# Optimization experiments

Measured on AMD Instinct MI355X. Metric: run time of the kernel, lower is better.

## Reference

```python
import jax, jax.numpy as jnp
import numpy as np

N_PARTITIONS = 16
EPS = 1e-5


def setup_inputs() -> dict:
    key = jax.random.key(0)
    ks = jax.random.split(key, 8)
    B, in_size = 4096, 4096
    d = in_size // N_PARTITIONS  # 256
    s = 1.0 / np.sqrt(d)
    return {
        "x": jax.random.normal(ks[0], (B, in_size), dtype=jnp.float32),
        "WQ_w": jax.random.normal(ks[1], (d, d), dtype=jnp.float32) * s,
        "WQ_b": jax.random.normal(ks[2], (d,), dtype=jnp.float32) * s,
        "WK_w": jax.random.normal(ks[3], (d, d), dtype=jnp.float32) * s,
        "WK_b": jax.random.normal(ks[4], (d,), dtype=jnp.float32) * s,
        "WV_w": jax.random.normal(ks[5], (d, d), dtype=jnp.float32) * s,
        "WV_b": jax.random.normal(ks[6], (d,), dtype=jnp.float32) * s,
        "bn_gamma": jnp.ones((in_size,), dtype=jnp.float32),
        "bn_beta": jnp.zeros((in_size,), dtype=jnp.float32),
    }


def reference(x, WQ_w, WQ_b, WK_w, WK_b, WV_w, WV_b, bn_gamma, bn_beta):
    B, in_size = x.shape
    p = N_PARTITIONS
    d = in_size // p
    scale = jnp.asarray(np.sqrt(d), dtype=x.dtype)

    # BatchNorm1d in training mode: batch statistics, biased variance
    mean = jnp.mean(x, axis=0)
    var = jnp.mean((x - mean) ** 2, axis=0)
    x_norm = (x - mean) * jax.lax.rsqrt(var + EPS) * bn_gamma + bn_beta

    # Split features into partitions: [B, p, d]; shared Linear per partition.
    xp = x_norm.reshape(B, p, d)
    # Torch loop builds Q[b, :, i] = WQ(x_part_i)[b]  ->  [B, d, p]
    Q = jnp.einsum('bpd,ed->bep', xp, WQ_w) + WQ_b[None, :, None]
    K = jnp.einsum('bpd,ed->bep', xp, WK_w) + WK_b[None, :, None]
    V = jnp.einsum('bpd,ed->bep', xp, WV_w) + WV_b[None, :, None]

    # bmm(Q, K^T): [B, d, d], softmax over last axis, bmm with V: [B, d, p]
    dot = jnp.einsum('bep,bfp->bef', Q, K) / scale
    attn = jax.nn.softmax(dot, axis=2)
    prod = jnp.einsum('bef,bfp->bep', attn, V)

    # torch.cat(prod[:, i] for i in range(d), dim=1) == row-major flatten of [B, d, p]
    out = prod.reshape(B, d * p) + x
    return out
```

## Files before the change

kernel.cpp:

```cpp
#include <hip/hip_runtime.h>
#include <hip/hip_bf16.h>
#include <stdint.h>

typedef __attribute__((ext_vector_type(8))) short short8;
typedef __attribute__((ext_vector_type(4))) short short4_t;
typedef __attribute__((ext_vector_type(4))) float f32x4;
typedef __attribute__((ext_vector_type(2))) unsigned int u32x2;
typedef __attribute__((ext_vector_type(4))) unsigned int u32x4;

union FragU { u32x4 u; short8 s; };
union Frag2U { u32x2 u; short4_t s; };

__device__ __forceinline__ unsigned short f2bf(float f) {
  union { float f; uint32_t u; } v; v.f = f;
  uint32_t u = v.u;
  return (unsigned short)((u + 0x7FFFu + ((u >> 16) & 1u)) >> 16);
}

__device__ __forceinline__ unsigned pk2(float a, float b) {
  return (unsigned)f2bf(a) | ((unsigned)f2bf(b) << 16);
}

__device__ __forceinline__ void gload_lds16(const void* g, void* l) {
  __builtin_amdgcn_global_load_lds(
      (const __attribute__((address_space(1))) unsigned int*)g,
      (__attribute__((address_space(3))) unsigned int*)l, 16, 0, 0);
}

#if defined(__has_builtin)
#if __has_builtin(__builtin_amdgcn_mfma_f32_16x16x16bf16_1k)
#define HAVE_MFMA16_BUILTIN 1
#endif
#endif

__device__ __forceinline__ f32x4 mfma16(u32x2 a, u32x2 b, f32x4 c) {
#ifdef HAVE_MFMA16_BUILTIN
  Frag2U ua, ub;
  ua.u = a; ub.u = b;
  return __builtin_amdgcn_mfma_f32_16x16x16bf16_1k(ua.s, ub.s, c, 0, 0, 0);
#else
  asm volatile("s_nop 1\n\t"
               "v_mfma_f32_16x16x16_bf16 %0, %1, %2, %0\n\t"
               "s_nop 7\n\t"
               "s_nop 7"
               : "+v"(c) : "v"(a), "v"(b));
  return c;
#endif
}

__global__ __launch_bounds__(256) void k_wconv(const float* __restrict__ WQ,
                                               const float* __restrict__ WK,
                                               const float* __restrict__ WV,
                                               unsigned short* __restrict__ Wbf) {
  int mat = blockIdx.x >> 5;
  int i = blockIdx.x & 31;
  const float* W = (mat == 0) ? WQ : ((mat == 1) ? WK : WV);
  int off = i * 2048 + threadIdx.x * 8;
  f32x4 v0 = *(const f32x4*)(W + off), v1 = *(const f32x4*)(W + off + 4);
  u32x4 pk;
  pk.x = pk2(v0.x, v0.y); pk.y = pk2(v0.z, v0.w);
  pk.z = pk2(v1.x, v1.y); pk.w = pk2(v1.z, v1.w);
  *(u32x4*)(Wbf + (size_t)mat * 65536 + off) = pk;
}

__global__ __launch_bounds__(256) void k_stats(const float* __restrict__ x,
                                               float* __restrict__ psum,
                                               float* __restrict__ psq) {
  int t = threadIdx.x;
  int cb = blockIdx.x & 3;
  int ck = blockIdx.x >> 2;
  int c0 = cb * 1024 + t * 4;
  f32x4 s = {0.f, 0.f, 0.f, 0.f}, q = {0.f, 0.f, 0.f, 0.f};
  const float* base = x + (size_t)ck * 64 * 4096 + c0;
#pragma unroll 4
  for (int r = 0; r < 64; ++r) {
    f32x4 v = *(const f32x4*)(base + (size_t)r * 4096);
    s += v;
    q += v * v;
  }
  *(f32x4*)(psum + (size_t)ck * 4096 + c0) = s;
  *(f32x4*)(psq + (size_t)ck * 4096 + c0) = q;
}

__global__ __launch_bounds__(256) void k_finalize(const float* __restrict__ psum,
                                                  const float* __restrict__ psq,
                                                  const float* __restrict__ gamma,
                                                  const float* __restrict__ beta,
                                                  float* __restrict__ An,
                                                  float* __restrict__ Bn) {
  int c = blockIdx.x * 256 + threadIdx.x;
  float s = 0.f, q = 0.f;
  for (int k = 0; k < 64; ++k) {
    s += psum[k * 4096 + c];
    q += psq[k * 4096 + c];
  }
  float mean = s * (1.0f / 4096.0f);
  float var = q * (1.0f / 4096.0f) - mean * mean;
  float a = gamma[c] * rsqrtf(var + 1e-5f);
  An[c] = a;
  Bn[c] = beta[c] - mean * a;
}

__global__ __launch_bounds__(256) void k_qkv(
    const float* __restrict__ x, const float* __restrict__ An, const float* __restrict__ Bn,
    const unsigned short* __restrict__ Wbf,
    const float* __restrict__ bQ, const float* __restrict__ bK, const float* __restrict__ bV,
    unsigned short* __restrict__ Qt, unsigned short* __restrict__ Kt,
    unsigned short* __restrict__ Vo) {
  __shared__ unsigned short Asm[64 * 256];
  int t = threadIdx.x;
  int mb = blockIdx.x;

  for (int i = 0; i < 8; ++i) {
    int m = i * 8 + (t >> 5);
    int k0 = (t & 31) * 8;
    size_t r = (size_t)(mb * 64 + m);
    const float* xs = x + r * 256 + k0;
    f32x4 v0 = *(const f32x4*)(xs), v1 = *(const f32x4*)(xs + 4);
    int c = ((int)(r & 15)) * 256 + k0;
    f32x4 a0 = *(const f32x4*)(An + c), a1 = *(const f32x4*)(An + c + 4);
    f32x4 b0 = *(const f32x4*)(Bn + c), b1 = *(const f32x4*)(Bn + c + 4);
    f32x4 n0 = v0 * a0 + b0, n1 = v1 * a1 + b1;
    u32x4 pk;
    pk.x = pk2(n0.x, n0.y); pk.y = pk2(n0.z, n0.w);
    pk.z = pk2(n1.x, n1.y); pk.w = pk2(n1.z, n1.w);
    int off = m * 512 + ((k0 * 2) ^ ((m & 7) << 4));
    *(u32x4*)((char*)Asm + off) = pk;
  }
  __syncthreads();

  int w = t >> 6, ln = t & 63, lr = ln & 15, g = ln >> 4;
  int wn = w * 64;

#pragma unroll
  for (int mat = 0; mat < 3; ++mat) {
    const unsigned short* W = Wbf + (size_t)mat * 65536;
    const float* bias = (mat == 0) ? bQ : ((mat == 1) ? bK : bV);
    float scale = (mat == 0) ? 0.0625f : 1.0f;

    f32x4 acc[4][4];
    f32x4 z4 = {0.f, 0.f, 0.f, 0.f};
#pragma unroll
    for (int a_ = 0; a_ < 4; ++a_)
#pragma unroll
      for (int b_ = 0; b_ < 4; ++b_) acc[a_][b_] = z4;

#pragma unroll
    for (int kk = 0; kk < 8; ++kk) {
      FragU af[4], bfr[4];
#pragma unroll
      for (int nt = 0; nt < 4; ++nt) {
        int n = wn + nt * 16 + lr;
        bfr[nt].u = *(const u32x4*)((const char*)W + (size_t)n * 512 + kk * 64 + g * 16);
      }
#pragma unroll
      for (int mt = 0; mt < 4; ++mt) {
        int m = mt * 16 + lr;
        af[mt].u = *(const u32x4*)((const char*)Asm + m * 512 + ((kk * 64 + g * 16) ^ ((m & 7) << 4)));
      }
#pragma unroll
      for (int mt = 0; mt < 4; ++mt)
#pragma unroll
        for (int nt = 0; nt < 4; ++nt)
          acc[mt][nt] = __builtin_amdgcn_mfma_f32_16x16x32_bf16(af[mt].s, bfr[nt].s, acc[mt][nt], 0, 0, 0);
    }

#pragma unroll
    for (int nt = 0; nt < 4; ++nt) {
      int ccol = wn + nt * 16 + lr;
      float bvs = bias[ccol] * scale;
#pragma unroll
      for (int mt = 0; mt < 4; ++mt) {
        int rbase = mb * 64 + mt * 16;
        int b_ = rbase >> 4;
#pragma unroll
        for (int rg = 0; rg < 4; ++rg) {
          int p_ = g * 4 + rg;
          unsigned short val = f2bf(acc[mt][nt][rg] * scale + bvs);
          if (mat < 2) {
            (mat == 0 ? Qt : Kt)[(size_t)b_ * 4096 + (size_t)ccol * 16 + p_] = val;
          } else {
            Vo[(size_t)(rbase + p_) * 256 + ccol] = val;
          }
        }
      }
    }
  }
}

#define LQT 0
#define LKT 8192
#define LVS 16384
#define LTOT 24576

__global__ __launch_bounds__(256, 3) void k_attn(
    const unsigned short* __restrict__ Qtg, const unsigned short* __restrict__ Ktg,
    const unsigned short* __restrict__ Vg, const float* __restrict__ x,
    float* __restrict__ out) {
  __shared__ char lds[LTOT];
  int b = blockIdx.x;
  int t = threadIdx.x;
  int w = t >> 6, ln = t & 63, lr = ln & 15, g = ln >> 4;

  for (int i = w; i < 24; i += 4) {
    const unsigned short* srcmat;
    unsigned srcbyte;
    int region;
    if (i < 8) {
      srcmat = Qtg;
      srcbyte = (unsigned)b * 8192 + i * 1024 + ln * 16;
      region = LQT + i * 1024;
    } else if (i < 16) {
      int ii = i - 8;
      srcmat = Ktg;
      srcbyte = (unsigned)b * 8192 + ii * 1024 + ln * 16;
      region = LKT + ii * 1024;
    } else {
      int ii = i - 16;
      srcmat = Vg;
      int d = ii * 1024 + ln * 16;
      int p = d >> 9;
      int cc = d & 511;
      srcbyte = (unsigned)b * 8192 + p * 512 + (unsigned)(cc ^ ((p & 7) << 4));
      region = LVS + ii * 1024;
    }
    gload_lds16((const char*)srcmat + srcbyte, &lds[region]);
  }
  __syncthreads();

  u32x2 qf[4];
#pragma unroll
  for (int nt = 0; nt < 4; ++nt)
    qf[nt] = *(const u32x2*)(&lds[LQT + (w * 64 + nt * 16 + lr) * 32 + g * 8]);

  f32x4 accT[4];
  float denp[4];
  f32x4 z4 = {0.f, 0.f, 0.f, 0.f};
#pragma unroll
  for (int nt = 0; nt < 4; ++nt) { accT[nt] = z4; denp[nt] = 0.f; }

  for (int c = 0; c < 8; ++c) {
#pragma unroll
    for (int mt_ = 0; mt_ < 2; ++mt_) {
      u32x2 kf = *(const u32x2*)(&lds[LKT + (c * 32 + mt_ * 16 + lr) * 32 + g * 8]);

      f32x4 st[4];
#pragma unroll
      for (int nt = 0; nt < 4; ++nt)
        st[nt] = mfma16(kf, qf[nt], z4);

      u32x2 vf = *(const u32x2*)(
          &lds[LVS + lr * 512 + ((c * 64 + mt_ * 32 + g * 8) ^ ((lr & 7) << 4))]);

#pragma unroll
      for (int nt = 0; nt < 4; ++nt) {
        float e0 = __expf(st[nt].x);
        float e1 = __expf(st[nt].y);
        float e2 = __expf(st[nt].z);
        float e3 = __expf(st[nt].w);
        denp[nt] += (e0 + e1) + (e2 + e3);
        u32x2 pB;
        pB.x = pk2(e0, e1);
        pB.y = pk2(e2, e3);
        accT[nt] = mfma16(vf, pB, accT[nt]);
      }
    }
  }

#pragma unroll
  for (int nt = 0; nt < 4; ++nt) {
    float v = denp[nt];
    v += __shfl_xor(v, 16);
    v += __shfl_xor(v, 32);
    denp[nt] = v;
  }

  size_t rowbase = (size_t)b * 4096;
#pragma unroll
  for (int nt = 0; nt < 4; ++nt) {
    int e = w * 64 + nt * 16 + lr;
    size_t col = (size_t)e * 16 + g * 4;
    float inv = 1.0f / denp[nt];
    f32x4 xr = *(const f32x4*)(x + rowbase + col);
    f32x4 o = accT[nt] * inv + xr;
    *(f32x4*)(out + rowbase + col) = o;
  }
}

extern "C" void kernel_launch(void* const* d_in, const int* in_sizes, int n_in,
                              void* d_out, int out_size, void* d_ws, size_t ws_size,
                              hipStream_t stream) {
  const float* x = (const float*)d_in[0];
  const float* WQ = (const float*)d_in[1];
  const float* bQ = (const float*)d_in[2];
  const float* WK = (const float*)d_in[3];
  const float* bK = (const float*)d_in[4];
  const float* WV = (const float*)d_in[5];
  const float* bV = (const float*)d_in[6];
  const float* gamma = (const float*)d_in[7];
  const float* beta = (const float*)d_in[8];
  float* out = (float*)d_out;
  char* ws = (char*)d_ws;

  float* psum = (float*)(ws);
  float* psq = (float*)(ws + (1 << 20));
  float* An = (float*)(ws + (2 << 20));
  float* Bn = (float*)(ws + (2 << 20) + (16 << 10));
  unsigned short* Wbf = (unsigned short*)(ws + (3 << 20));
  unsigned short* Qt = (unsigned short*)(ws + (size_t)(4 << 20));
  unsigned short* Kt = (unsigned short*)(ws + (size_t)(4 << 20) + (32u << 20));
  unsigned short* Vo = (unsigned short*)(ws + (size_t)(4 << 20) + (64u << 20));

  hipLaunchKernelGGL(k_wconv, dim3(96), dim3(256), 0, stream, WQ, WK, WV, Wbf);
  hipLaunchKernelGGL(k_stats, dim3(256), dim3(256), 0, stream, x, psum, psq);
  hipLaunchKernelGGL(k_finalize, dim3(16), dim3(256), 0, stream, psum, psq, gamma, beta, An, Bn);
  hipLaunchKernelGGL(k_qkv, dim3(1024), dim3(256), 0, stream, x, An, Bn,
                     Wbf, bQ, bK, bV, Qt, Kt, Vo);
  hipLaunchKernelGGL(k_attn, dim3(4096), dim3(256), 0, stream, Qt, Kt, Vo, x, out);
}
```

Baseline: 153.2 us.

## Fuse QKV projection and attention into one per-wave kernel

Merges the QKV projection and attention kernels so each wave handles one batch row, keeping Q, K and V fragments in registers instead of writing them to global memory and reloading them through LDS. This removes the Q/K/V intermediate round trip (about 24 MB written and read back) and one kernel launch. The softmax exponent now uses exp2 with log2(e) folded into the Q scale. Each wave now reads all three weight matrices from global/L2 with no LDS sharing, and the register pressure is heavy (16-entry fragment arrays), which may cause spills or low occupancy.

```diff
diff --git a/kernel.cpp b/kernel.cpp
--- a/kernel.cpp
+++ b/kernel.cpp
@@ -21,17 +21,22 @@
   return (unsigned)f2bf(a) | ((unsigned)f2bf(b) << 16);
 }
 
-__device__ __forceinline__ void gload_lds16(const void* g, void* l) {
-  __builtin_amdgcn_global_load_lds(
-      (const __attribute__((address_space(1))) unsigned int*)g,
-      (__attribute__((address_space(3))) unsigned int*)l, 16, 0, 0);
-}
-
 #if defined(__has_builtin)
 #if __has_builtin(__builtin_amdgcn_mfma_f32_16x16x16bf16_1k)
 #define HAVE_MFMA16_BUILTIN 1
 #endif
-#endif
+#if __has_builtin(__builtin_amdgcn_exp2f)
+#define HAVE_EXP2_BUILTIN 1
+#endif
+#endif
+
+__device__ __forceinline__ float fexp2(float x) {
+#ifdef HAVE_EXP2_BUILTIN
+  return __builtin_amdgcn_exp2f(x);
+#else
+  return exp2f(x);
+#endif
+}
 
 __device__ __forceinline__ f32x4 mfma16(u32x2 a, u32x2 b, f32x4 c) {
 #ifdef HAVE_MFMA16_BUILTIN
@@ -101,186 +106,135 @@
   Bn[c] = beta[c] - mean * a;
 }
 
-__global__ __launch_bounds__(256) void k_qkv(
+__global__ __launch_bounds__(256, 2) void k_fused(
     const float* __restrict__ x, const float* __restrict__ An, const float* __restrict__ Bn,
     const unsigned short* __restrict__ Wbf,
     const float* __restrict__ bQ, const float* __restrict__ bK, const float* __restrict__ bV,
-    unsigned short* __restrict__ Qt, unsigned short* __restrict__ Kt,
-    unsigned short* __restrict__ Vo) {
-  __shared__ unsigned short Asm[64 * 256];
+    float* __restrict__ out) {
   int t = threadIdx.x;
-  int mb = blockIdx.x;
-
-  for (int i = 0; i < 8; ++i) {
-    int m = i * 8 + (t >> 5);
-    int k0 = (t & 31) * 8;
-    size_t r = (size_t)(mb * 64 + m);
-    const float* xs = x + r * 256 + k0;
-    f32x4 v0 = *(const f32x4*)(xs), v1 = *(const f32x4*)(xs + 4);
-    int c = ((int)(r & 15)) * 256 + k0;
+  int w = t >> 6, ln = t & 63, lr = ln & 15, g = ln >> 4;
+  int b = blockIdx.x * 4 + w;
+  const float* xrow = x + (size_t)b * 4096;
+
+  f32x4 z4 = {0.f, 0.f, 0.f, 0.f};
+
+  FragU af[8];
+#pragma unroll
+  for (int kk = 0; kk < 8; ++kk) {
+    int dd = kk * 32 + g * 8;
+    int c = lr * 256 + dd;
+    f32x4 v0 = *(const f32x4*)(xrow + c), v1 = *(const f32x4*)(xrow + c + 4);
     f32x4 a0 = *(const f32x4*)(An + c), a1 = *(const f32x4*)(An + c + 4);
     f32x4 b0 = *(const f32x4*)(Bn + c), b1 = *(const f32x4*)(Bn + c + 4);
     f32x4 n0 = v0 * a0 + b0, n1 = v1 * a1 + b1;
-    u32x4 pk;
-    pk.x = pk2(n0.x, n0.y); pk.y = pk2(n0.z, n0.w);
-    pk.z = pk2(n1.x, n1.y); pk.w = pk2(n1.z, n1.w);
-    int off = m * 512 + ((k0 * 2) ^ ((m & 7) << 4));
-    *(u32x4*)((char*)Asm + off) = pk;
-  }
-  __syncthreads();
-
-  int w = t >> 6, ln = t & 63, lr = ln & 15, g = ln >> 4;
-  int wn = w * 64;
-
-#pragma unroll
-  for (int mat = 0; mat < 3; ++mat) {
-    const unsigned short* W = Wbf + (size_t)mat * 65536;
-    const float* bias = (mat == 0) ? bQ : ((mat == 1) ? bK : bV);
-    float scale = (mat == 0) ? 0.0625f : 1.0f;
-
-    f32x4 acc[4][4];
-    f32x4 z4 = {0.f, 0.f, 0.f, 0.f};
-#pragma unroll
-    for (int a_ = 0; a_ < 4; ++a_)
-#pragma unroll
-      for (int b_ = 0; b_ < 4; ++b_) acc[a_][b_] = z4;
-
+    af[kk].u.x = pk2(n0.x, n0.y);
+    af[kk].u.y = pk2(n0.z, n0.w);
+    af[kk].u.z = pk2(n1.x, n1.y);
+    af[kk].u.w = pk2(n1.z, n1.w);
+  }
+
+  const char* WQp = (const char*)Wbf;
+  const char* WKp = (const char*)(Wbf + 65536);
+  const char* WVp = (const char*)(Wbf + 131072);
+
+  u32x2 qf[16];
+  {
+    f32x4 acc[16];
+#pragma unroll
+    for (int nt = 0; nt < 16; ++nt) acc[nt] = z4;
 #pragma unroll
     for (int kk = 0; kk < 8; ++kk) {
-      FragU af[4], bfr[4];
-#pragma unroll
-      for (int nt = 0; nt < 4; ++nt) {
-        int n = wn + nt * 16 + lr;
-        bfr[nt].u = *(const u32x4*)((const char*)W + (size_t)n * 512 + kk * 64 + g * 16);
+#pragma unroll
+      for (int nt = 0; nt < 16; ++nt) {
+        FragU bfr;
+        bfr.u = *(const u32x4*)(WQp + (size_t)(nt * 16 + lr) * 512 + kk * 64 + g * 16);
+        acc[nt] = __builtin_amdgcn_mfma_f32_16x16x32_bf16(af[kk].s, bfr.s, acc[nt], 0, 0, 0);
       }
-#pragma unroll
-      for (int mt = 0; mt < 4; ++mt) {
-        int m = mt * 16 + lr;
-        af[mt].u = *(const u32x4*)((const char*)Asm + m * 512 + ((kk * 64 + g * 16) ^ ((m & 7) << 4)));
+    }
+    const float QS = 0.0625f * 1.44269504088896f;
+#pragma unroll
+    for (int nt = 0; nt < 16; ++nt) {
+      float bq = bQ[nt * 16 + lr];
+      qf[nt].x = pk2((acc[nt][0] + bq) * QS, (acc[nt][1] + bq) * QS);
+      qf[nt].y = pk2((acc[nt][2] + bq) * QS, (acc[nt][3] + bq) * QS);
+    }
+  }
+
+  u32x2 kf[16];
+  {
+    f32x4 acc[16];
+#pragma unroll
+    for (int nt = 0; nt < 16; ++nt) acc[nt] = z4;
+#pragma unroll
+    for (int kk = 0; kk < 8; ++kk) {
+#pragma unroll
+      for (int nt = 0; nt < 16; ++nt) {
+        FragU bfr;
+        bfr.u = *(const u32x4*)(WKp + (size_t)(nt * 16 + lr) * 512 + kk * 64 + g * 16);
+        acc[nt] = __builtin_amdgcn_mfma_f32_16x16x32_bf16(af[kk].s, bfr.s, acc[nt], 0, 0, 0);
       }
-#pragma unroll
-      for (int mt = 0; mt < 4; ++mt)
-#pragma unroll
-        for (int nt = 0; nt < 4; ++nt)
-          acc[mt][nt] = __builtin_amdgcn_mfma_f32_16x16x32_bf16(af[mt].s, bfr[nt].s, acc[mt][nt], 0, 0, 0);
-    }
-
-#pragma unroll
-    for (int nt = 0; nt < 4; ++nt) {
-      int ccol = wn + nt * 16 + lr;
-      float bvs = bias[ccol] * scale;
-#pragma unroll
-      for (int mt = 0; mt < 4; ++mt) {
-        int rbase = mb * 64 + mt * 16;
-        int b_ = rbase >> 4;
-#pragma unroll
-        for (int rg = 0; rg < 4; ++rg) {
-          int p_ = g * 4 + rg;
-          unsigned short val = f2bf(acc[mt][nt][rg] * scale + bvs);
-          if (mat < 2) {
-            (mat == 0 ? Qt : Kt)[(size_t)b_ * 4096 + (size_t)ccol * 16 + p_] = val;
-          } else {
-            Vo[(size_t)(rbase + p_) * 256 + ccol] = val;
-          }
-        }
+    }
+#pragma unroll
+    for (int nt = 0; nt < 16; ++nt) {
+      float bk = bK[nt * 16 + lr];
+      kf[nt].x = pk2(acc[nt][0] + bk, acc[nt][1] + bk);
+      kf[nt].y = pk2(acc[nt][2] + bk, acc[nt][3] + bk);
+    }
+  }
+
+  u32x2 vf[16];
+  {
+    f32x4 acc[16];
+#pragma unroll
+    for (int mt = 0; mt < 16; ++mt) acc[mt] = z4;
+#pragma unroll
+    for (int kk = 0; kk < 8; ++kk) {
+#pragma unroll
+      for (int mt = 0; mt < 16; ++mt) {
+        FragU wf;
+        wf.u = *(const u32x4*)(WVp + (size_t)(mt * 16 + lr) * 512 + kk * 64 + g * 16);
+        acc[mt] = __builtin_amdgcn_mfma_f32_16x16x32_bf16(wf.s, af[kk].s, acc[mt], 0, 0, 0);
       }
     }
-  }
-}
-
-#define LQT 0
-#define LKT 8192
-#define LVS 16384
-#define LTOT 24576
-
-__global__ __launch_bounds__(256, 3) void k_attn(
-    const unsigned short* __restrict__ Qtg, const unsigned short* __restrict__ Ktg,
-    const unsigned short* __restrict__ Vg, const float* __restrict__ x,
-    float* __restrict__ out) {
-  __shared__ char lds[LTOT];
-  int b = blockIdx.x;
-  int t = threadIdx.x;
-  int w = t >> 6, ln = t & 63, lr = ln & 15, g = ln >> 4;
-
-  for (int i = w; i < 24; i += 4) {
-    const unsigned short* srcmat;
-    unsigned srcbyte;
-    int region;
-    if (i < 8) {
-      srcmat = Qtg;
-      srcbyte = (unsigned)b * 8192 + i * 1024 + ln * 16;
-      region = LQT + i * 1024;
-    } else if (i < 16) {
-      int ii = i - 8;
-      srcmat = Ktg;
-      srcbyte = (unsigned)b * 8192 + ii * 1024 + ln * 16;
-      region = LKT + ii * 1024;
-    } else {
-      int ii = i - 16;
-      srcmat = Vg;
-      int d = ii * 1024 + ln * 16;
-      int p = d >> 9;
-      int cc = d & 511;
-      srcbyte = (unsigned)b * 8192 + p * 512 + (unsigned)(cc ^ ((p & 7) << 4));
-      region = LVS + ii * 1024;
-    }
-    gload_lds16((const char*)srcmat + srcbyte, &lds[region]);
-  }
-  __syncthreads();
-
-  u32x2 qf[4];
-#pragma unroll
-  for (int nt = 0; nt < 4; ++nt)
-    qf[nt] = *(const u32x2*)(&lds[LQT + (w * 64 + nt * 16 + lr) * 32 + g * 8]);
-
-  f32x4 accT[4];
-  float denp[4];
-  f32x4 z4 = {0.f, 0.f, 0.f, 0.f};
-#pragma unroll
-  for (int nt = 0; nt < 4; ++nt) { accT[nt] = z4; denp[nt] = 0.f; }
-
-  for (int c = 0; c < 8; ++c) {
-#pragma unroll
-    for (int mt_ = 0; mt_ < 2; ++mt_) {
-      u32x2 kf = *(const u32x2*)(&lds[LKT + (c * 32 + mt_ * 16 + lr) * 32 + g * 8]);
-
-      f32x4 st[4];
-#pragma unroll
-      for (int nt = 0; nt < 4; ++nt)
-        st[nt] = mfma16(kf, qf[nt], z4);
-
-      u32x2 vf = *(const u32x2*)(
-          &lds[LVS + lr * 512 + ((c * 64 + mt_ * 32 + g * 8) ^ ((lr & 7) << 4))]);
-
-#pragma unroll
-      for (int nt = 0; nt < 4; ++nt) {
-        float e0 = __expf(st[nt].x);
-        float e1 = __expf(st[nt].y);
-        float e2 = __expf(st[nt].z);
-        float e3 = __expf(st[nt].w);
-        denp[nt] += (e0 + e1) + (e2 + e3);
-        u32x2 pB;
-        pB.x = pk2(e0, e1);
-        pB.y = pk2(e2, e3);
-        accT[nt] = mfma16(vf, pB, accT[nt]);
-      }
-    }
-  }
-
-#pragma unroll
-  for (int nt = 0; nt < 4; ++nt) {
+#pragma unroll
+    for (int mt = 0; mt < 16; ++mt) {
+      int f0 = mt * 16 + g * 4;
+      f32x4 bv4 = *(const f32x4*)(bV + f0);
+      vf[mt].x = pk2(acc[mt][0] + bv4.x, acc[mt][1] + bv4.y);
+      vf[mt].y = pk2(acc[mt][2] + bv4.z, acc[mt][3] + bv4.w);
+    }
+  }
+
+  f32x4 accT[16];
+  float denp[16];
+#pragma unroll
+  for (int nt = 0; nt < 16; ++nt) { accT[nt] = z4; denp[nt] = 0.f; }
+
+#pragma unroll
+  for (int c2 = 0; c2 < 16; ++c2) {
+#pragma unroll
+    for (int nt = 0; nt < 16; ++nt) {
+      f32x4 st = mfma16(kf[c2], qf[nt], z4);
+      float p0 = fexp2(st[0]);
+      float p1 = fexp2(st[1]);
+      float p2 = fexp2(st[2]);
+      float p3 = fexp2(st[3]);
+      denp[nt] += (p0 + p1) + (p2 + p3);
+      u32x2 pB;
+      pB.x = pk2(p0, p1);
+      pB.y = pk2(p2, p3);
+      accT[nt] = mfma16(vf[c2], pB, accT[nt]);
+    }
+  }
+
+  size_t rowbase = (size_t)b * 4096;
+#pragma unroll
+  for (int nt = 0; nt < 16; ++nt) {
     float v = denp[nt];
     v += __shfl_xor(v, 16);
     v += __shfl_xor(v, 32);
-    denp[nt] = v;
-  }
-
-  size_t rowbase = (size_t)b * 4096;
-#pragma unroll
-  for (int nt = 0; nt < 4; ++nt) {
-    int e = w * 64 + nt * 16 + lr;
-    size_t col = (size_t)e * 16 + g * 4;
-    float inv = 1.0f / denp[nt];
+    float inv = 1.0f / v;
+    size_t col = (size_t)(nt * 16 + lr) * 16 + g * 4;
     f32x4 xr = *(const f32x4*)(x + rowbase + col);
     f32x4 o = accT[nt] * inv + xr;
     *(f32x4*)(out + rowbase + col) = o;
@@ -307,14 +261,10 @@
   float* An = (float*)(ws + (2 << 20));
   float* Bn = (float*)(ws + (2 << 20) + (16 << 10));
   unsigned short* Wbf = (unsigned short*)(ws + (3 << 20));
-  unsigned short* Qt = (unsigned short*)(ws + (size_t)(4 << 20));
-  unsigned short* Kt = (unsigned short*)(ws + (size_t)(4 << 20) + (32u << 20));
-  unsigned short* Vo = (unsigned short*)(ws + (size_t)(4 << 20) + (64u << 20));
 
   hipLaunchKernelGGL(k_wconv, dim3(96), dim3(256), 0, stream, WQ, WK, WV, Wbf);
   hipLaunchKernelGGL(k_stats, dim3(256), dim3(256), 0, stream, x, psum, psq);
   hipLaunchKernelGGL(k_finalize, dim3(16), dim3(256), 0, stream, psum, psq, gamma, beta, An, Bn);
-  hipLaunchKernelGGL(k_qkv, dim3(1024), dim3(256), 0, stream, x, An, Bn,
-                     Wbf, bQ, bK, bV, Qt, Kt, Vo);
-  hipLaunchKernelGGL(k_attn, dim3(4096), dim3(256), 0, stream, Qt, Kt, Vo, x, out);
-}
+  hipLaunchKernelGGL(k_fused, dim3(1024), dim3(256), 0, stream, x, An, Bn,
+                     Wbf, bQ, bK, bV, out);
+}
```

After: 302.0 us. 1.97x slower.

## Retile QKV projection into 128x128 output tiles with LDS-staged weights

Applied to the files above, without the earlier changes.

The fused QKV kernel becomes a generic tiled GEMM. Each block now computes one 128x128 output tile for one of six column blocks, instead of producing all three 768-column projections for 64 rows. Weight tiles are staged into LDS with global-to-LDS loads and a swizzled layout rather than read straight from global memory, and Q/K results are written with packed 8-byte stores. In exchange, each block re-reads and re-normalizes its x rows once per column block, so x traffic grows about sixfold, and each block now uses 80KB of LDS. Separately, the attention kernel's occupancy hint is raised from 3 to 4 blocks per CU.

```diff
diff --git a/kernel.cpp b/kernel.cpp
--- a/kernel.cpp
+++ b/kernel.cpp
@@ -101,20 +101,24 @@
   Bn[c] = beta[c] - mean * a;
 }
 
-__global__ __launch_bounds__(256) void k_qkv(
+__global__ __launch_bounds__(256) void k_gemm(
     const float* __restrict__ x, const float* __restrict__ An, const float* __restrict__ Bn,
     const unsigned short* __restrict__ Wbf,
     const float* __restrict__ bQ, const float* __restrict__ bK, const float* __restrict__ bV,
     unsigned short* __restrict__ Qt, unsigned short* __restrict__ Kt,
     unsigned short* __restrict__ Vo) {
-  __shared__ unsigned short Asm[64 * 256];
+  __shared__ char lds[81920];
   int t = threadIdx.x;
-  int mb = blockIdx.x;
-
-  for (int i = 0; i < 8; ++i) {
+  int bid = blockIdx.x;
+  int nb = bid >> 9;
+  int mb = bid & 511;
+  int w = t >> 6, ln = t & 63, lr = ln & 15, g = ln >> 4;
+  int wm = (w >> 1) * 64, wn = (w & 1) * 64;
+
+  for (int i = 0; i < 16; ++i) {
     int m = i * 8 + (t >> 5);
     int k0 = (t & 31) * 8;
-    size_t r = (size_t)(mb * 64 + m);
+    size_t r = (size_t)(mb * 128 + m);
     const float* xs = x + r * 256 + k0;
     f32x4 v0 = *(const f32x4*)(xs), v1 = *(const f32x4*)(xs + 4);
     int c = ((int)(r & 15)) * 256 + k0;
@@ -125,64 +129,72 @@
     pk.x = pk2(n0.x, n0.y); pk.y = pk2(n0.z, n0.w);
     pk.z = pk2(n1.x, n1.y); pk.w = pk2(n1.z, n1.w);
     int off = m * 512 + ((k0 * 2) ^ ((m & 7) << 4));
-    *(u32x4*)((char*)Asm + off) = pk;
+    *(u32x4*)(&lds[off]) = pk;
   }
   __syncthreads();
 
-  int w = t >> 6, ln = t & 63, lr = ln & 15, g = ln >> 4;
-  int wn = w * 64;
-
-#pragma unroll
-  for (int mat = 0; mat < 3; ++mat) {
-    const unsigned short* W = Wbf + (size_t)mat * 65536;
-    const float* bias = (mat == 0) ? bQ : ((mat == 1) ? bK : bV);
-    float scale = (mat == 0) ? 0.0625f : 1.0f;
-
-    f32x4 acc[4][4];
-    f32x4 z4 = {0.f, 0.f, 0.f, 0.f};
-#pragma unroll
-    for (int a_ = 0; a_ < 4; ++a_)
-#pragma unroll
-      for (int b_ = 0; b_ < 4; ++b_) acc[a_][b_] = z4;
-
-#pragma unroll
-    for (int kk = 0; kk < 8; ++kk) {
-      FragU af[4], bfr[4];
-#pragma unroll
-      for (int nt = 0; nt < 4; ++nt) {
-        int n = wn + nt * 16 + lr;
-        bfr[nt].u = *(const u32x4*)((const char*)W + (size_t)n * 512 + kk * 64 + g * 16);
-      }
-#pragma unroll
-      for (int mt = 0; mt < 4; ++mt) {
-        int m = mt * 16 + lr;
-        af[mt].u = *(const u32x4*)((const char*)Asm + m * 512 + ((kk * 64 + g * 16) ^ ((m & 7) << 4)));
-      }
+  const char* Bbase = (const char*)Wbf + (size_t)(nb * 128) * 512;
+
+  f32x4 acc[4][4];
+  f32x4 z4 = {0.f, 0.f, 0.f, 0.f};
+#pragma unroll
+  for (int a_ = 0; a_ < 4; ++a_)
+#pragma unroll
+    for (int b_ = 0; b_ < 4; ++b_) acc[a_][b_] = z4;
+
+  for (int kb = 0; kb < 4; ++kb) {
+#pragma unroll
+    for (int pc = 0; pc < 4; ++pc) {
+      int ob = pc * 4096 + w * 1024;
+      int o = ob + ln * 16;
+      int r = o >> 7;
+      int cc = o & 127;
+      int sw = cc ^ ((r & 7) << 4);
+      gload_lds16(Bbase + (size_t)r * 512 + kb * 128 + sw, &lds[65536 + ob]);
+    }
+    __syncthreads();
+
+#pragma unroll
+    for (int kk2 = 0; kk2 < 2; ++kk2) {
+      int szB = (kk2 * 64 + g * 16) ^ ((lr & 7) << 4);
+      int szA = (kb * 128 + kk2 * 64 + g * 16) ^ ((lr & 7) << 4);
+      FragU afr[4], bfr[4];
 #pragma unroll
       for (int mt = 0; mt < 4; ++mt)
+        afr[mt].u = *(const u32x4*)(&lds[(wm + mt * 16 + lr) * 512 + szA]);
+#pragma unroll
+      for (int nt = 0; nt < 4; ++nt)
+        bfr[nt].u = *(const u32x4*)(&lds[65536 + (wn + nt * 16 + lr) * 128 + szB]);
+#pragma unroll
+      for (int mt = 0; mt < 4; ++mt)
 #pragma unroll
         for (int nt = 0; nt < 4; ++nt)
-          acc[mt][nt] = __builtin_amdgcn_mfma_f32_16x16x32_bf16(af[mt].s, bfr[nt].s, acc[mt][nt], 0, 0, 0);
-    }
-
-#pragma unroll
-    for (int nt = 0; nt < 4; ++nt) {
-      int ccol = wn + nt * 16 + lr;
-      float bvs = bias[ccol] * scale;
-#pragma unroll
-      for (int mt = 0; mt < 4; ++mt) {
-        int rbase = mb * 64 + mt * 16;
-        int b_ = rbase >> 4;
-#pragma unroll
-        for (int rg = 0; rg < 4; ++rg) {
-          int p_ = g * 4 + rg;
-          unsigned short val = f2bf(acc[mt][nt][rg] * scale + bvs);
-          if (mat < 2) {
-            (mat == 0 ? Qt : Kt)[(size_t)b_ * 4096 + (size_t)ccol * 16 + p_] = val;
-          } else {
-            Vo[(size_t)(rbase + p_) * 256 + ccol] = val;
-          }
-        }
+          acc[mt][nt] = __builtin_amdgcn_mfma_f32_16x16x32_bf16(afr[mt].s, bfr[nt].s, acc[mt][nt], 0, 0, 0);
+    }
+    __syncthreads();
+  }
+
+  int mat = nb >> 1;
+  const float* bias = (mat == 0) ? bQ : ((mat == 1) ? bK : bV);
+  float scale = (mat == 0) ? 0.0625f : 1.0f;
+#pragma unroll
+  for (int nt = 0; nt < 4; ++nt) {
+    int e = (nb & 1) * 128 + wn + nt * 16 + lr;
+    float bvs = bias[e] * scale;
+#pragma unroll
+    for (int mt = 0; mt < 4; ++mt) {
+      int xrow0 = mb * 128 + wm + mt * 16;
+      if (mat < 2) {
+        unsigned short* Out = (mat == 0) ? Qt : Kt;
+        int b_ = xrow0 >> 4;
+        u32x2 pk;
+        pk.x = pk2(acc[mt][nt][0] * scale + bvs, acc[mt][nt][1] * scale + bvs);
+        pk.y = pk2(acc[mt][nt][2] * scale + bvs, acc[mt][nt][3] * scale + bvs);
+        *(u32x2*)(Out + (size_t)b_ * 4096 + (size_t)e * 16 + g * 4) = pk;
+      } else {
+#pragma unroll
+        for (int rg = 0; rg < 4; ++rg)
+          Vo[(size_t)(xrow0 + g * 4 + rg) * 256 + e] = f2bf(acc[mt][nt][rg] + bvs);
       }
     }
   }
@@ -193,7 +205,7 @@
 #define LVS 16384
 #define LTOT 24576
 
-__global__ __launch_bounds__(256, 3) void k_attn(
+__global__ __launch_bounds__(256, 4) void k_attn(
     const unsigned short* __restrict__ Qtg, const unsigned short* __restrict__ Ktg,
     const unsigned short* __restrict__ Vg, const float* __restrict__ x,
     float* __restrict__ out) {
@@ -314,7 +326,7 @@
   hipLaunchKernelGGL(k_wconv, dim3(96), dim3(256), 0, stream, WQ, WK, WV, Wbf);
   hipLaunchKernelGGL(k_stats, dim3(256), dim3(256), 0, stream, x, psum, psq);
   hipLaunchKernelGGL(k_finalize, dim3(16), dim3(256), 0, stream, psum, psq, gamma, beta, An, Bn);
-  hipLaunchKernelGGL(k_qkv, dim3(1024), dim3(256), 0, stream, x, An, Bn,
+  hipLaunchKernelGGL(k_gemm, dim3(3072), dim3(256), 0, stream, x, An, Bn,
                      Wbf, bQ, bK, bV, Qt, Kt, Vo);
   hipLaunchKernelGGL(k_attn, dim3(4096), dim3(256), 0, stream, Qt, Kt, Vo, x, out);
 }
```

Result: slower. 181.7 us (+18.6%).
